# Optimization experiments

Hardware: AMD Instinct MI355X
Metric: run time of the kernel (lower is better)

The kernel has to match this reference:

```python
import jax, jax.numpy as jnp
import numpy as np

AUX_LOSS_COEFF = 0.03125  # config.aux_loss_coeff


def setup_inputs() -> dict:
    key = jax.random.key(0)
    k0, k1 = jax.random.split(key, 2)
    B, T, d, m = 2, 2048, 2048, 16384
    activations = jax.random.normal(k0, (B, T, d), dtype=jnp.float32)
    # kaiming-uniform-ish init, then unit-norm rows (as in _initialize_weights)
    W_enc = jax.random.normal(k1, (m, d), dtype=jnp.float32)
    W_enc = W_enc / (jnp.linalg.norm(W_enc, axis=1, keepdims=True) + 1e-8)
    b_enc = jnp.zeros((m,), dtype=jnp.float32)
    W_emb = W_enc.T  # tied init: W_emb.weight = W_enc.weight.T, shape [d, m]
    steps_since_active = jnp.zeros((m,), dtype=jnp.int32)  # buffer, starts at 0
    return {
        "activations": activations,
        "W_enc": W_enc,
        "b_enc": b_enc,
        "W_emb": W_emb,
        "steps_since_active": steps_since_active,
        "topk": 64,
        "dead_window": 1000,
    }


def reference(activations, W_enc, b_enc, W_emb, steps_since_active, topk, dead_window):
    B, T, d = activations.shape
    m = W_enc.shape[0]
    # pre_act = W_enc(activations)  -> [B, T, m]
    pre_act = jnp.einsum("btd,md->btm", activations, W_enc) + b_enc
    # top-k over concept dim
    top_vals, top_idx = jax.lax.top_k(pre_act, topk)  # [B, T, k]
    # sparse = zeros scatter top_vals at top_idx along last dim
    flat_idx = top_idx.reshape(-1, topk)   # [B*T, k]
    flat_vals = top_vals.reshape(-1, topk)
    rows = jnp.arange(flat_idx.shape[0])[:, None]
    sparse = (
        jnp.zeros((flat_idx.shape[0], m), dtype=pre_act.dtype)
        .at[rows, flat_idx]
        .set(flat_vals)
        .reshape(B, T, m)
    )
    # encoded = W_emb(sparse) -> [B, T, d]
    encoded = jnp.einsum("btm,dm->btd", sparse, W_emb)
    # aux loss on dead concepts (dead_mask all False at init -> 0.0)
    dead_mask = (steps_since_active >= dead_window).astype(pre_act.dtype)  # [m]
    n_dead = jnp.sum(dead_mask)
    denom = jnp.maximum(n_dead * B * T, 1.0)
    dead_mean = jnp.sum(pre_act * dead_mask) / denom
    aux_loss = jnp.where(n_dead > 0, -dead_mean * AUX_LOSS_COEFF, jnp.zeros((), pre_act.dtype))
    return encoded, aux_loss
```

## Files before the change

kernel.cpp:

```cpp
#include <hip/hip_runtime.h>
#include <cfloat>
#include <climits>


typedef __attribute__((ext_vector_type(8))) short short8;
typedef __attribute__((ext_vector_type(4))) float f32x4;

#define NC      96
#define KFIN    64
#define TAU     1e-3f
#define AUXC    0.03125f
#define MCONC   16384
#define DDIM    2048
#define CAP     768

__device__ __forceinline__ ushort f2bf(float f) {
  unsigned u = __float_as_uint(f);
  u += 0x7fff + ((u >> 16) & 1);
  return (ushort)(u >> 16);
}
__device__ __forceinline__ float bf2f(ushort h) {
  return __uint_as_float(((unsigned)h) << 16);
}

__global__ void k_init(float* dead_sum, int* n_dead, int* wl_count) {
  *dead_sum = 0.f;
  *n_dead = 0;
  *wl_count = 0;
}

__global__ void k_count_dead(const int* __restrict__ steps, const int* __restrict__ dw,
                             int m, int* __restrict__ n_dead) {
  int i = blockIdx.x * blockDim.x + threadIdx.x;
  if (i < m && steps[i] >= *dw) atomicAdd(n_dead, 1);
}

__global__ void k_final(const float* __restrict__ ds, const int* __restrict__ nd,
                        float* __restrict__ outp, float BT) {
  int n = *nd;
  float denom = fmaxf((float)n * BT, 1.0f);
  outp[0] = (n > 0) ? -((*ds) / denom) * AUXC : 0.0f;
}

__global__ __launch_bounds__(256)
void k_prep(const float* __restrict__ srcA, ushort* __restrict__ dstA, int totA,
            const float* __restrict__ srcB, ushort* __restrict__ dstB, int totB,
            int K,
            const float* __restrict__ Wemb, ushort* __restrict__ WembT,
            int d, int m, int nstage) {
  __shared__ float tile[32][33];
  const int b = blockIdx.x;
  if (b < nstage) {
    int idx = b * 256 + threadIdx.x;
    const float* src;
    ushort* dst;
    int t;
    if (idx < totA) { src = srcA; dst = dstA; t = idx; }
    else if (idx < totA + totB) { src = srcB; dst = dstB; t = idx - totA; }
    else return;
    int nch = K >> 5;
    int row = t / nch, c = t - row * nch;
    const float* s = src + (size_t)row * K + c * 32;
    float f[32];
#pragma unroll
    for (int q = 0; q < 8; ++q) *(float4*)&f[q * 4] = *(const float4*)(s + q * 4);
    ushort hi[32];
    float lof[32];
#pragma unroll
    for (int e = 0; e < 32; ++e) {
      hi[e] = f2bf(f[e]);
      lof[e] = f[e] - bf2f(hi[e]);
    }
    ushort* dd = dst + (size_t)row * ((size_t)K * 2) + c * 64;
#pragma unroll
    for (int q = 0; q < 4; ++q) {
      short8 o;
#pragma unroll
      for (int e = 0; e < 8; ++e) o[e] = (short)hi[q * 8 + e];
      *(short8*)(dd + q * 8) = o;
    }
#pragma unroll
    for (int q = 0; q < 4; ++q) {
      short8 o;
#pragma unroll
      for (int e = 0; e < 8; ++e) o[e] = (short)f2bf(lof[q * 8 + e]);
      *(short8*)(dd + 32 + q * 8) = o;
    }
    return;
  }
  const int tb = b - nstage;
  const int nmb = m >> 5;
  const int mb = (tb % nmb) * 32, db = (tb / nmb) * 32;
  const int tx = threadIdx.x & 31, ty = threadIdx.x >> 5;
#pragma unroll
  for (int i = 0; i < 32; i += 8)
    tile[ty + i][tx] = Wemb[(size_t)(db + ty + i) * m + mb + tx];
  __syncthreads();
#pragma unroll
  for (int i = 0; i < 32; i += 8)
    WembT[(size_t)(mb + ty + i) * d + db + tx] = f2bf(tile[tx][ty + i]);
}

__device__ __forceinline__ void gload16(const void* g, void* l) {
  __builtin_amdgcn_global_load_lds((const __attribute__((address_space(1))) void*)g,
                                   (__attribute__((address_space(3))) void*)l, 16, 0, 0);
}

__global__ __launch_bounds__(256, 3)
void k_gemm3(const ushort* __restrict__ Ast, const ushort* __restrict__ Bst,
             const float* __restrict__ bias, float* __restrict__ C,
             int row0, int K, int m, int nbm) {
  __shared__ ushort As[128 * 64];
  __shared__ ushort Bs[128 * 64];
  const int tid = threadIdx.x;
  const int lane = tid & 63, w = tid >> 6;
  const int wm = w >> 1, wn = w & 1;

  const int nbn = m >> 7;
  const int nwg = nbm * nbn;
  const int q = nwg >> 3, r = nwg & 7;
  const int x = blockIdx.x & 7, i0 = blockIdx.x >> 3;
  const int wg = (x < r) ? x * (q + 1) + i0 : r * (q + 1) + (x - r) * q + i0;
  const int bm = wg / nbn, bn = wg % nbn;

  const size_t K2 = (size_t)K * 2;
  const int nch = K >> 5;

  const int gr = lane >> 3;
  const int swz = (((lane & 7) ^ gr) << 3);
  const size_t arow0 = (size_t)(row0 + bm * 128);
  const size_t brow0 = (size_t)(bn * 128);

  f32x4 acc[4][4];
#pragma unroll
  for (int i = 0; i < 4; ++i)
#pragma unroll
    for (int j = 0; j < 4; ++j) acc[i][j] = (f32x4)(0.f);

  const int kg = lane >> 4;
  const int j7 = lane & 7;
  const int sh = ((kg ^ j7) << 3);
  const int rbase = (lane & 15) * 64;

  for (int c = 0; c < nch; ++c) {
#pragma unroll
    for (int t = 0; t < 4; ++t) {
      int i = w * 4 + t;
      int rr = i * 8 + gr;
      gload16(Ast + (arow0 + rr) * K2 + (size_t)c * 64 + swz, (void*)(As + i * 512));
      gload16(Bst + (brow0 + rr) * K2 + (size_t)c * 64 + swz, (void*)(Bs + i * 512));
    }
    __syncthreads();
    short8 ah[4], al[4], bh[4], bl[4];
#pragma unroll
    for (int f = 0; f < 4; ++f) {
      const ushort* pa = As + (wm * 64 + f * 16) * 64 + rbase;
      ah[f] = *(const short8*)(pa + sh);
      al[f] = *(const short8*)(pa + (sh ^ 32));
      const ushort* pb = Bs + (wn * 64 + f * 16) * 64 + rbase;
      bh[f] = *(const short8*)(pb + sh);
      bl[f] = *(const short8*)(pb + (sh ^ 32));
    }
#pragma unroll
    for (int fm = 0; fm < 4; ++fm)
#pragma unroll
      for (int fn = 0; fn < 4; ++fn) {
        acc[fm][fn] = __builtin_amdgcn_mfma_f32_16x16x32_bf16(ah[fm], bh[fn], acc[fm][fn], 0, 0, 0);
        acc[fm][fn] = __builtin_amdgcn_mfma_f32_16x16x32_bf16(ah[fm], bl[fn], acc[fm][fn], 0, 0, 0);
        acc[fm][fn] = __builtin_amdgcn_mfma_f32_16x16x32_bf16(al[fm], bh[fn], acc[fm][fn], 0, 0, 0);
      }
    __syncthreads();
  }

  const int orow = bm * 128 + wm * 64;
  const int ocol = bn * 128 + wn * 64;
#pragma unroll
  for (int fn = 0; fn < 4; ++fn) {
    float bb = bias[ocol + fn * 16 + (lane & 15)];
#pragma unroll
    for (int fm = 0; fm < 4; ++fm) {
      int rb = orow + fm * 16 + (lane >> 4) * 4;
#pragma unroll
      for (int rr = 0; rr < 4; ++rr)
        __builtin_nontemporal_store(acc[fm][fn][rr] + bb,
            &C[(size_t)(rb + rr) * m + ocol + fn * 16 + (lane & 15)]);
    }
  }
}

__global__ __launch_bounds__(256)
void k_topk(const float* __restrict__ preact, int row0,
            const int* __restrict__ steps, const int* __restrict__ dw,
            const int* __restrict__ topk_d,
            float* __restrict__ cvals, int* __restrict__ cidx,
            float* __restrict__ dead_sum,
            int* __restrict__ rowflag, int* __restrict__ wl, int* __restrict__ wl_count,
            float* __restrict__ tvals, int* __restrict__ tidx) {
  __shared__ float dred[4];
  __shared__ float wmx[4], wmn[4];
  __shared__ float sm1[4], sm2[4];
  __shared__ int scnt;
  __shared__ int pos;
  __shared__ float cval_s[CAP];
  __shared__ int cidx_s[CAP];
  __shared__ float vk1_s, vk_s;
  __shared__ int flag_s;
  const int tid = threadIdx.x;
  const int lane = tid & 63;
  const int grow = row0 + blockIdx.x;
  const float* pr = preact + (size_t)blockIdx.x * MCONC;

  int kt = *topk_d;
  if (kt > KFIN) kt = KFIN;
  if (kt < 1) kt = 1;

  float v[64];
#pragma unroll
  for (int c = 0; c < 16; ++c) {
    const f32x4* p4 = (const f32x4*)(pr + (size_t)c * 1024 + tid * 4);
    f32x4 t4 = __builtin_nontemporal_load(p4);
    v[c * 4 + 0] = t4[0]; v[c * 4 + 1] = t4[1];
    v[c * 4 + 2] = t4[2]; v[c * 4 + 3] = t4[3];
  }

  int dwv = *dw;
  float ds = 0.f;
#pragma unroll
  for (int c = 0; c < 16; ++c) {
    int4 st = *(const int4*)(steps + c * 1024 + tid * 4);
    if (st.x >= dwv) ds += v[c * 4 + 0];
    if (st.y >= dwv) ds += v[c * 4 + 1];
    if (st.z >= dwv) ds += v[c * 4 + 2];
    if (st.w >= dwv) ds += v[c * 4 + 3];
  }
  for (int off = 32; off; off >>= 1) ds += __shfl_down(ds, off);
  if (lane == 0) dred[tid >> 6] = ds;

  float mx = -FLT_MAX, mn = FLT_MAX, s1 = 0.f, s2 = 0.f;
#pragma unroll
  for (int i = 0; i < 64; ++i) {
    mx = fmaxf(mx, v[i]); mn = fminf(mn, v[i]);
    s1 += v[i]; s2 = fmaf(v[i], v[i], s2);
  }
  for (int off = 32; off; off >>= 1) {
    mx = fmaxf(mx, __shfl_xor(mx, off));
    mn = fminf(mn, __shfl_xor(mn, off));
    s1 += __shfl_xor(s1, off);
    s2 += __shfl_xor(s2, off);
  }
  if (lane == 0) { wmx[tid >> 6] = mx; wmn[tid >> 6] = mn; sm1[tid >> 6] = s1; sm2[tid >> 6] = s2; }
  __syncthreads();
  if (tid == 0) {
    float t = dred[0] + dred[1] + dred[2] + dred[3];
    if (t != 0.f) atomicAdd(dead_sum, t);
  }
  float row_mx = fmaxf(fmaxf(wmx[0], wmx[1]), fmaxf(wmx[2], wmx[3]));
  float row_mn = fminf(fminf(wmn[0], wmn[1]), fminf(wmn[2], wmn[3]));
  float T1 = sm1[0] + sm1[1] + sm1[2] + sm1[3];
  float T2 = sm2[0] + sm2[1] + sm2[2] + sm2[3];
  float mu = T1 * (1.f / 16384.f);
  float var = fmaxf(T2 * (1.f / 16384.f) - mu * mu, 0.f);
  float mid = mu + 2.0f * sqrtf(var);

  float lo = row_mn - 1.0f, hi = row_mx;
  float t = lo;
  bool found = false;
  for (int it = 0; it < 23 && !found; ++it) {
    __syncthreads();
    if (tid == 0) scnt = 0;
    __syncthreads();
    int cl = 0;
#pragma unroll
    for (int i = 0; i < 64; ++i) cl += (v[i] > mid);
    for (int off = 32; off; off >>= 1) cl += __shfl_xor(cl, off);
    if (lane == 0) atomicAdd(&scnt, cl);
    __syncthreads();
    int cnt = scnt;
    if (cnt >= NC && cnt <= CAP) { t = mid; found = true; }
    else if (cnt < NC) hi = mid;
    else lo = mid;
    mid = 0.5f * (lo + hi);
  }
  if (!found) t = lo;

  __syncthreads();
  if (tid == 0) pos = 0;
  __syncthreads();
#pragma unroll
  for (int i = 0; i < 64; ++i) {
    if (v[i] > t) {
      int p = atomicAdd(&pos, 1);
      if (p < CAP) {
        cval_s[p] = v[i];
        cidx_s[p] = ((i >> 2) << 10) | (tid << 2) | (i & 3);
      }
    }
  }
  __syncthreads();
  int Cn = pos < CAP ? pos : CAP;

  int rnk[3];
  float mvv[3];
  int mii[3];
#pragma unroll
  for (int jj = 0; jj < 3; ++jj) {
    int j = tid + jj * 256;
    rnk[jj] = INT_MAX;
    if (j < Cn) {
      float my = cval_s[j];
      int myidx = cidx_s[j];
      int rank = 0;
      for (int c = 0; c < Cn; ++c) {
        float o = cval_s[c];
        rank += (o > my) || (o == my && cidx_s[c] < myidx);
      }
      rnk[jj] = rank; mvv[jj] = my; mii[jj] = myidx;
      if (rank < NC) {
        cvals[(size_t)grow * NC + rank] = my;
        cidx[(size_t)grow * NC + rank] = myidx;
      }
      if (rank == kt - 1) vk1_s = my;
      if (rank == kt)     vk_s  = my;
    }
  }
  __syncthreads();
  if (tid == 0) {
    int f = (vk1_s - vk_s < TAU) ? 1 : 0;
    rowflag[grow] = f;
    flag_s = f;
    if (f) { int p = atomicAdd(wl_count, 1); wl[p] = grow; }
  }
  __syncthreads();
  if (!flag_s) {
#pragma unroll
    for (int jj = 0; jj < 3; ++jj) {
      if (rnk[jj] < kt) {
        tvals[(size_t)grow * KFIN + rnk[jj]] = mvv[jj];
        tidx[(size_t)grow * KFIN + rnk[jj]] = mii[jj];
      }
    }
  }
}

__global__ __launch_bounds__(256)
void k_dots(const int* __restrict__ wl, const int* __restrict__ wl_count,
            const int* __restrict__ cidx, const float* __restrict__ act,
            const float* __restrict__ Wenc, const float* __restrict__ bias,
            double* __restrict__ dv, int d) {
  __shared__ float arow[DDIM];
  const int total = (*wl_count) * 8;
  const int lane = threadIdx.x & 63, w = threadIdx.x >> 6;
  for (int b = blockIdx.x; b < total; b += gridDim.x) {
    const int row = wl[b >> 3], part = b & 7;
    __syncthreads();
    for (int i = threadIdx.x; i < d; i += 256) arow[i] = act[(size_t)row * d + i];
    __syncthreads();
#pragma unroll
    for (int cc = 0; cc < 3; ++cc) {
      int c = part * 12 + w * 3 + cc;
      int ci = cidx[(size_t)row * NC + c];
      const float* wrow = Wenc + (size_t)ci * d;
      double s = 0.0;
      for (int i = lane; i < d; i += 64)
        s += (double)arow[i] * (double)wrow[i];
      for (int off = 32; off; off >>= 1) s += __shfl_down(s, off);
      if (lane == 0) dv[(size_t)row * NC + c] = s + (double)bias[ci];
    }
  }
}

__global__ __launch_bounds__(128)
void k_select(const float* __restrict__ cvals, const int* __restrict__ cidx,
              const int* __restrict__ rowflag, const double* __restrict__ dv,
              const int* __restrict__ topk_d,
              float* __restrict__ tvals, int* __restrict__ tidx) {
  const int row = blockIdx.x, tid = threadIdx.x;
  if (!rowflag[row]) return;
  int kt = *topk_d;
  if (kt > KFIN) kt = KFIN;
  if (kt < 1) kt = 1;
  __shared__ double sdv[NC];
  if (tid < NC) sdv[tid] = dv[(size_t)row * NC + tid];
  __syncthreads();
  if (tid < NC) {
    double my = sdv[tid];
    int rank = 0;
#pragma unroll 8
    for (int c = 0; c < NC; ++c) {
      double v = sdv[c];
      rank += (v > my) || (v == my && c < tid);
    }
    if (rank < kt) {
      tvals[(size_t)row * KFIN + rank] = cvals[(size_t)row * NC + tid];
      tidx[(size_t)row * KFIN + rank] = cidx[(size_t)row * NC + tid];
    }
  }
}

__global__ __launch_bounds__(256)
void k_decode_t(const float* __restrict__ tvals, const int* __restrict__ tidx,
                const int* __restrict__ topk_d, const ushort* __restrict__ Wt,
                float* __restrict__ out, int d) {
  __shared__ float sv[KFIN];
  __shared__ int si[KFIN];
  const int row = blockIdx.x, tid = threadIdx.x;
  int kt = *topk_d;
  if (kt > KFIN) kt = KFIN;
  if (tid < kt) {
    sv[tid] = tvals[(size_t)row * KFIN + tid];
    si[tid] = tidx[(size_t)row * KFIN + tid];
  }
  __syncthreads();
  for (int base = tid * 8; base < d; base += 2048) {
    float a0 = 0, a1 = 0, a2 = 0, a3 = 0, a4 = 0, a5 = 0, a6 = 0, a7 = 0;
#pragma unroll 4
    for (int j = 0; j < kt; ++j) {
      float vv = sv[j];
      short8 wv = *(const short8*)(Wt + (size_t)si[j] * d + base);
      a0 = fmaf(vv, bf2f((ushort)wv[0]), a0);
      a1 = fmaf(vv, bf2f((ushort)wv[1]), a1);
      a2 = fmaf(vv, bf2f((ushort)wv[2]), a2);
      a3 = fmaf(vv, bf2f((ushort)wv[3]), a3);
      a4 = fmaf(vv, bf2f((ushort)wv[4]), a4);
      a5 = fmaf(vv, bf2f((ushort)wv[5]), a5);
      a6 = fmaf(vv, bf2f((ushort)wv[6]), a6);
      a7 = fmaf(vv, bf2f((ushort)wv[7]), a7);
    }
    float* o = out + (size_t)row * d + base;
    *(float4*)o = make_float4(a0, a1, a2, a3);
    *(float4*)(o + 4) = make_float4(a4, a5, a6, a7);
  }
}

__global__ __launch_bounds__(256)
void k_decode_g(const float* __restrict__ tvals, const int* __restrict__ tidx,
                const int* __restrict__ topk_d, const float* __restrict__ Wemb,
                float* __restrict__ out, int d, int m) {
  __shared__ float sv[KFIN];
  __shared__ int si[KFIN];
  const int row = blockIdx.x, tid = threadIdx.x;
  int kt = *topk_d;
  if (kt > KFIN) kt = KFIN;
  if (tid < kt) {
    sv[tid] = tvals[(size_t)row * KFIN + tid];
    si[tid] = tidx[(size_t)row * KFIN + tid];
  }
  __syncthreads();
  for (int base = tid * 8; base < d; base += 2048) {
    float acc[8] = {0, 0, 0, 0, 0, 0, 0, 0};
    for (int j = 0; j < kt; ++j) {
      float vv = sv[j];
      int ix = si[j];
#pragma unroll
      for (int e = 0; e < 8; ++e)
        acc[e] = fmaf(vv, Wemb[(size_t)(base + e) * m + ix], acc[e]);
    }
    float* o = out + (size_t)row * d + base;
    *(float4*)o = *(float4*)&acc[0];
    *(float4*)(o + 4) = *(float4*)&acc[4];
  }
}

extern "C" void kernel_launch(void* const* d_in, const int* in_sizes, int n_in,
                              void* d_out, int out_size, void* d_ws, size_t ws_size,
                              hipStream_t stream) {
  const float* act   = (const float*)d_in[0];
  const float* Wenc  = (const float*)d_in[1];
  const float* benc  = (const float*)d_in[2];
  const float* Wemb  = (const float*)d_in[3];
  const int*   steps = (const int*)d_in[4];
  const int*   topk  = (const int*)d_in[5];
  const int*   dwin  = (const int*)d_in[6];
  const int m = in_sizes[2];
  const int d = in_sizes[1] / m;
  const int rows = in_sizes[0] / d;
  float* out = (float*)d_out;

  char* ws = (char*)d_ws;
  float* dead_sum = (float*)ws;
  int*   n_dead   = (int*)(ws + 8);
  int*   wl_count = (int*)(ws + 16);
  size_t off = 256;
  float* cvals = (float*)(ws + off); off += (size_t)rows * NC * 4;
  int*   cidx  = (int*)(ws + off);   off += (size_t)rows * NC * 4;
  float* tvals = (float*)(ws + off); off += (size_t)rows * KFIN * 4;
  int*   tidx  = (int*)(ws + off);   off += (size_t)rows * KFIN * 4;
  int*   rowflag = (int*)(ws + off); off += (size_t)rows * 4;
  int*   wl      = (int*)(ws + off); off += (size_t)rows * 4;
  double* dv     = (double*)(ws + off); off += (size_t)rows * NC * 8;
  ushort* Ast  = (ushort*)(ws + off); off += (size_t)rows * d * 4;
  ushort* Bst  = (ushort*)(ws + off); off += (size_t)m * d * 4;

  const size_t wembT_bytes = (size_t)m * d * sizeof(ushort);
  const size_t row_bytes = (size_t)m * sizeof(float);
  size_t avail = (ws_size > off) ? ws_size - off : 0;

  ushort* WembT = nullptr;
  if (avail >= wembT_bytes + 128 * row_bytes) {
    WembT = (ushort*)(ws + off);
    off += wembT_bytes;
    avail -= wembT_bytes;
  }
  int chunk = (int)(avail / row_bytes);
  if (chunk > rows) chunk = rows;
  chunk &= ~127;
  if (chunk < 128) chunk = 128;
  float* preact = (float*)(ws + off);

  k_init<<<1, 1, 0, stream>>>(dead_sum, n_dead, wl_count);
  k_count_dead<<<(m + 255) / 256, 256, 0, stream>>>(steps, dwin, m, n_dead);

  int totA = rows * (d >> 5);
  int totB = m * (d >> 5);
  int nstage = (totA + totB + 255) / 256;
  int ntrans = WembT ? (m / 32) * (d / 32) : 0;
  k_prep<<<nstage + ntrans, 256, 0, stream>>>(act, Ast, totA, Wenc, Bst, totB, d,
                                              Wemb, WembT, d, m, nstage);

  for (int r0 = 0; r0 < rows; r0 += chunk) {
    int cr = rows - r0;
    if (cr > chunk) cr = chunk;
    int nbm = cr / 128;
    int nwg = nbm * (m / 128);
    k_gemm3<<<nwg, 256, 0, stream>>>(Ast, Bst, benc, preact, r0, d, m, nbm);
    k_topk<<<cr, 256, 0, stream>>>(preact, r0, steps, dwin, topk,
                                   cvals, cidx, dead_sum,
                                   rowflag, wl, wl_count, tvals, tidx);
  }

  k_dots<<<rows, 256, 0, stream>>>(wl, wl_count, cidx, act, Wenc, benc, dv, d);
  k_select<<<rows, 128, 0, stream>>>(cvals, cidx, rowflag, dv, topk, tvals, tidx);

  if (WembT) {
    k_decode_t<<<rows, 256, 0, stream>>>(tvals, tidx, topk, WembT, out, d);
  } else {
    k_decode_g<<<rows, 256, 0, stream>>>(tvals, tidx, topk, Wemb, out, d, m);
  }

  k_final<<<1, 1, 0, stream>>>(dead_sum, n_dead, out + (size_t)rows * d, (float)rows);
}
```

Measured before the change: 1.256 ms.

## Enlarge GEMM tile to 256x128 with 8 waves and triple-buffered LDS prefetch

The encoder GEMM now uses 512-thread workgroups that compute 256x128 output tiles. LDS is triple-buffered so global-to-LDS loads for chunk j+2 are issued while chunk j is computed, with explicit vmcnt waits and raw s_barrier in place of __syncthreads. MFMA priority is raised during the compute phase, and the host chunking is adjusted to multiples of 256 rows. This aims to hide memory latency and increase reuse per block, at the cost of higher LDS use (about 144KB per block) and lower occupancy.

```diff
diff --git a/kernel.cpp b/kernel.cpp
--- a/kernel.cpp
+++ b/kernel.cpp
@@ -106,12 +106,12 @@
                                    (__attribute__((address_space(3))) void*)l, 16, 0, 0);
 }
 
-__global__ __launch_bounds__(256, 3)
+__global__ __launch_bounds__(512, 2)
 void k_gemm3(const ushort* __restrict__ Ast, const ushort* __restrict__ Bst,
              const float* __restrict__ bias, float* __restrict__ C,
              int row0, int K, int m, int nbm) {
-  __shared__ ushort As[128 * 64];
-  __shared__ ushort Bs[128 * 64];
+  __shared__ ushort As[3][256 * 64];
+  __shared__ ushort Bs[3][128 * 64];
   const int tid = threadIdx.x;
   const int lane = tid & 63, w = tid >> 6;
   const int wm = w >> 1, wn = w & 1;
@@ -128,7 +128,7 @@
 
   const int gr = lane >> 3;
   const int swz = (((lane & 7) ^ gr) << 3);
-  const size_t arow0 = (size_t)(row0 + bm * 128);
+  const size_t arow0 = (size_t)(row0 + bm * 256);
   const size_t brow0 = (size_t)(bn * 128);
 
   f32x4 acc[4][4];
@@ -142,25 +142,47 @@
   const int sh = ((kg ^ j7) << 3);
   const int rbase = (lane & 15) * 64;
 
-  for (int c = 0; c < nch; ++c) {
+  auto STAGE = [&](int buf, int c) {
 #pragma unroll
     for (int t = 0; t < 4; ++t) {
       int i = w * 4 + t;
       int rr = i * 8 + gr;
-      gload16(Ast + (arow0 + rr) * K2 + (size_t)c * 64 + swz, (void*)(As + i * 512));
-      gload16(Bst + (brow0 + rr) * K2 + (size_t)c * 64 + swz, (void*)(Bs + i * 512));
-    }
-    __syncthreads();
+      gload16(Ast + (arow0 + rr) * K2 + (size_t)c * 64 + swz, (void*)(As[buf] + i * 512));
+    }
+#pragma unroll
+    for (int t = 0; t < 2; ++t) {
+      int i = w * 2 + t;
+      int rr = i * 8 + gr;
+      gload16(Bst + (brow0 + rr) * K2 + (size_t)c * 64 + swz, (void*)(Bs[buf] + i * 512));
+    }
+  };
+
+  STAGE(0, 0);
+  if (nch > 1) STAGE(1, 1);
+
+  for (int j = 0; j < nch; ++j) {
+    const int cur = j % 3;
+    if (j + 2 < nch) {
+      STAGE((j + 2) % 3, j + 2);
+      asm volatile("s_waitcnt vmcnt(12)" ::: "memory");
+    } else if (j + 1 < nch) {
+      asm volatile("s_waitcnt vmcnt(6)" ::: "memory");
+    } else {
+      asm volatile("s_waitcnt vmcnt(0)" ::: "memory");
+    }
+    asm volatile("s_barrier" ::: "memory");
+
     short8 ah[4], al[4], bh[4], bl[4];
 #pragma unroll
     for (int f = 0; f < 4; ++f) {
-      const ushort* pa = As + (wm * 64 + f * 16) * 64 + rbase;
+      const ushort* pa = As[cur] + (wm * 64 + f * 16) * 64 + rbase;
       ah[f] = *(const short8*)(pa + sh);
       al[f] = *(const short8*)(pa + (sh ^ 32));
-      const ushort* pb = Bs + (wn * 64 + f * 16) * 64 + rbase;
+      const ushort* pb = Bs[cur] + (wn * 64 + f * 16) * 64 + rbase;
       bh[f] = *(const short8*)(pb + sh);
       bl[f] = *(const short8*)(pb + (sh ^ 32));
     }
+    __builtin_amdgcn_s_setprio(1);
 #pragma unroll
     for (int fm = 0; fm < 4; ++fm)
 #pragma unroll
@@ -169,10 +191,11 @@
         acc[fm][fn] = __builtin_amdgcn_mfma_f32_16x16x32_bf16(ah[fm], bl[fn], acc[fm][fn], 0, 0, 0);
         acc[fm][fn] = __builtin_amdgcn_mfma_f32_16x16x32_bf16(al[fm], bh[fn], acc[fm][fn], 0, 0, 0);
       }
-    __syncthreads();
-  }
-
-  const int orow = bm * 128 + wm * 64;
+    __builtin_amdgcn_s_setprio(0);
+    asm volatile("s_barrier" ::: "memory");
+  }
+
+  const int orow = bm * 256 + wm * 64;
   const int ocol = bn * 128 + wn * 64;
 #pragma unroll
   for (int fn = 0; fn < 4; ++fn) {
@@ -496,15 +519,15 @@
   size_t avail = (ws_size > off) ? ws_size - off : 0;
 
   ushort* WembT = nullptr;
-  if (avail >= wembT_bytes + 128 * row_bytes) {
+  if (avail >= wembT_bytes + 256 * row_bytes) {
     WembT = (ushort*)(ws + off);
     off += wembT_bytes;
     avail -= wembT_bytes;
   }
   int chunk = (int)(avail / row_bytes);
   if (chunk > rows) chunk = rows;
-  chunk &= ~127;
-  if (chunk < 128) chunk = 128;
+  chunk &= ~255;
+  if (chunk < 256) chunk = 256;
   float* preact = (float*)(ws + off);
 
   k_init<<<1, 1, 0, stream>>>(dead_sum, n_dead, wl_count);
@@ -520,9 +543,9 @@
   for (int r0 = 0; r0 < rows; r0 += chunk) {
     int cr = rows - r0;
     if (cr > chunk) cr = chunk;
-    int nbm = cr / 128;
+    int nbm = cr / 256;
     int nwg = nbm * (m / 128);
-    k_gemm3<<<nwg, 256, 0, stream>>>(Ast, Bst, benc, preact, r0, d, m, nbm);
+    k_gemm3<<<nwg, 512, 0, stream>>>(Ast, Bst, benc, preact, r0, d, m, nbm);
     k_topk<<<cr, 256, 0, stream>>>(preact, r0, steps, dwin, topk,
                                    cvals, cidx, dead_sum,
                                    rowflag, wl, wl_count, tvals, tidx);
```

Result: slower. 1.451 ms (+15.4%).
